# Performance work log

Measured on AMD Instinct MI355X. Metric: run time of the kernel, lower is better.

## Reference

```python
import jax, jax.numpy as jnp
import numpy as np

B, C, H = 256, 5, 13
N_AGENTS = 8192
N_EDGES = 262144
ACT = 21


def setup_inputs() -> dict:
    key = jax.random.key(0)
    ks = jax.random.split(key, 20)
    inp = {
        "x": jax.random.normal(ks[0], (B, C, H, H), jnp.float32),
        "x_msg": jax.random.normal(ks[1], (N_AGENTS,), jnp.float32),
        "edge_index": jax.random.randint(ks[2], (N_EDGES, 2), 0, N_AGENTS, jnp.int64 if jax.config.jax_enable_x64 else jnp.int32),
        "action": jax.random.randint(ks[3], (B,), 0, ACT, jnp.int32),
        # params (orthogonal init approximated by scaled normal; math identical)
        "conv1_w": jax.random.normal(ks[4], (32, 5, 3, 3), jnp.float32) * 0.1,
        "conv1_b": jnp.zeros((32,), jnp.float32),
        "conv2_w": jax.random.normal(ks[5], (64, 32, 3, 3), jnp.float32) * 0.05,
        "conv2_b": jnp.zeros((64,), jnp.float32),
        "fc_w": jax.random.normal(ks[6], (512, 1024), jnp.float32) * 0.03,
        "fc_b": jnp.zeros((512,), jnp.float32),
        "fc_mu_w": jax.random.normal(ks[7], (ACT, 512), jnp.float32) * 0.01,
        "fc_mu_b": jnp.zeros((ACT,), jnp.float32),
        "msg_w": jax.random.normal(ks[8], (N_AGENTS, 512), jnp.float32) * 0.01,
        "msg_b": jnp.zeros((N_AGENTS,), jnp.float32),
        "gcn1_w": jax.random.normal(ks[9], (2, 16), jnp.float32) * 0.5,
        "gcn1_b": jnp.zeros((16,), jnp.float32),
        "gcn2_w": jax.random.normal(ks[10], (16, N_AGENTS), jnp.float32) * 0.1,
        "gcn2_b": jnp.zeros((N_AGENTS,), jnp.float32),
    }
    return inp


def _gcn_norm(edge_index, n):
    # add self-loops; edge_index is (E,2) [src, dst]
    loops = jnp.arange(n, dtype=edge_index.dtype)
    src = jnp.concatenate([edge_index[:, 0], loops])
    dst = jnp.concatenate([edge_index[:, 1], loops])
    deg = jax.ops.segment_sum(jnp.ones_like(src, jnp.float32), dst, num_segments=n)
    dinv = jnp.where(deg > 0, jax.lax.rsqrt(deg), 0.0)
    norm = dinv[src] * dinv[dst]  # [E+n]
    return src, dst, norm


def _gcn_conv(h, src, dst, norm, W, b, n):
    hw = h @ W  # [n, out]
    out = jax.ops.segment_sum(norm[:, None] * hw[src], dst, num_segments=n)
    return out + b


def reference(x, x_msg, edge_index, action, conv1_w, conv1_b, conv2_w, conv2_b,
              fc_w, fc_b, fc_mu_w, fc_mu_b, msg_w, msg_b,
              gcn1_w, gcn1_b, gcn2_w, gcn2_b):
    dn = ("NCHW", "OIHW", "NCHW")
    h = jax.lax.conv_general_dilated(x, conv1_w, (2, 2), "VALID", dimension_numbers=dn)
    h = jax.nn.relu(h + conv1_b[None, :, None, None])  # [B,32,6,6]
    h = jax.lax.conv_general_dilated(h, conv2_w, (1, 1), "VALID", dimension_numbers=dn)
    h = jax.nn.relu(h + conv2_b[None, :, None, None])  # [B,64,4,4]
    h = h.reshape(h.shape[0], -1)  # [B,1024], torch NCHW flatten order
    hidden = jax.nn.relu(h @ fc_w.T + fc_b)  # [B,512]

    logits = hidden @ fc_mu_w.T + fc_mu_b            # [B,21]
    actor_encoding = hidden @ msg_w.T + msg_b        # [B,N]

    # Categorical log_prob / entropy for the given action
    logp = jax.nn.log_softmax(logits, axis=-1)
    log_prob = jnp.take_along_axis(logp, action[:, None], axis=1)[:, 0]
    entropy = -jnp.sum(jnp.exp(logp) * logp, axis=-1)

    # GNN message branch (eval mode: dropout is identity)
    feats = jnp.stack([x_msg, actor_encoding[0]], axis=0).T  # [N,2]
    n = feats.shape[0]
    src, dst, norm = _gcn_norm(edge_index, n)
    g = jax.nn.relu(_gcn_conv(feats, src, dst, norm, gcn1_w, gcn1_b, n))  # [N,16]
    g = _gcn_conv(g, src, dst, norm, gcn2_w, gcn2_b, n)                    # [N,N]
    msg_out = jax.nn.log_softmax(g, axis=1).mean(axis=1)                   # [N]

    return (action, msg_out, log_prob, entropy)
```

## Files before the change

kernel.cpp:

```cpp
#include <hip/hip_runtime.h>
#include <hip/hip_bf16.h>

#define NB 256
#define NACT 21
#define NA 8192
#define NE 262144
#define CSR_CAP 128
#define LOG2E 1.44269504f

#if __has_builtin(__builtin_amdgcn_exp2f)
#define EXP2F(x) __builtin_amdgcn_exp2f(x)
#else
#define EXP2F(x) exp2f(x)
#endif

typedef __attribute__((ext_vector_type(8))) short short8;
typedef __attribute__((ext_vector_type(4))) float float4v;

__device__ inline float wsum64(float v) {
#pragma unroll
  for (int m = 32; m > 0; m >>= 1) v += __shfl_xor(v, m, 64);
  return v;
}

__device__ inline unsigned short f2bf(float f) {
  union { __hip_bfloat16 h; unsigned short u; } cv;
  cv.h = __float2bfloat16(f);
  return cv.u;
}

__global__ __launch_bounds__(512) void k_init(int* cnt) {
  int i = blockIdx.x * 512 + threadIdx.x;
  cnt[i] = 0;
}

__global__ __launch_bounds__(512, 2) void k_pc(
    const int* __restrict__ edges, const float* __restrict__ fcw,
    const float* __restrict__ g2w, const float* __restrict__ g2b,
    unsigned short* fcwbf, unsigned short* w2t, float* wpart, int* cnt, int* csr,
    const float* __restrict__ x, const float* __restrict__ c1w, const float* __restrict__ c1b,
    const float* __restrict__ c2w, const float* __restrict__ c2b, unsigned short* h1024bf) {
  __shared__ float sm[8109];
  int t = threadIdx.x;
  if (blockIdx.x < 512) {
    float (*red)[17] = (float(*)[17])sm;
    float* b2s = sm + 272;
    int blk = blockIdx.x;
    {
      int e = blk * 512 + t;
      int s = edges[2 * e], d = edges[2 * e + 1];
      int slot = atomicAdd(&cnt[d], 1);
      if (slot < CSR_CAP) csr[d * CSR_CAP + slot] = s;
    }
    {
      int base = (blk * 512 + t) * 2;
      float2 v = *(const float2*)&fcw[base];
      fcwbf[base + 0] = f2bf(v.x);
      fcwbf[base + 1] = f2bf(v.y);
    }
    {
      if (t < 256) {
        int jj = t >> 4, k = t & 15;
        int j = blk * 16 + jj;
        float w = g2w[k * 8192 + j];
        w2t[j * 16 + k] = f2bf(w);
        red[jj][k] = w;
      }
      if (t < 16) b2s[t] = g2b[blk * 16 + t];
      __syncthreads();
      if (t < 16) {
        float s = 0.0f;
#pragma unroll
        for (int q = 0; q < 16; q++) s += red[q][t];
        wpart[blk * 17 + t] = s;
      } else if (t == 16) {
        float s = 0.0f;
#pragma unroll
        for (int q = 0; q < 16; q++) s += b2s[q];
        wpart[blk * 17 + 16] = s;
      }
    }
  } else {
    float* xs = sm;
    float* w1s = sm + 845;
    float* c1s = sm + 2285;
    float* w2s = sm + 3437;
    int blk = blockIdx.x - 512;
    for (int i = t; i < 845; i += 512) xs[i] = x[blk * 845 + i];
    for (int i = t; i < 1440; i += 512) w1s[i] = c1w[i];
    __syncthreads();
    for (int idx = t; idx < 1152; idx += 512) {
      int oc = idx / 36, p = idx - oc * 36;
      int oy = p / 6, ox = p - oy * 6;
      float acc = c1b[oc];
      const float* wp = &w1s[oc * 45];
#pragma unroll
      for (int ic = 0; ic < 5; ic++)
#pragma unroll
        for (int ky = 0; ky < 3; ky++)
#pragma unroll
          for (int kx = 0; kx < 3; kx++)
            acc += xs[ic * 169 + (oy * 2 + ky) * 13 + ox * 2 + kx] * wp[ic * 9 + ky * 3 + kx];
      c1s[idx] = fmaxf(acc, 0.0f);
    }
    int p = t & 15, oc2 = t >> 4;
    int oy = p >> 2, ox = p & 3;
    float a0 = c2b[oc2 * 2 + 0], a1 = c2b[oc2 * 2 + 1];
    for (int icb = 0; icb < 32; icb += 8) {
      __syncthreads();
      for (int i = t; i < 4608; i += 512) {
        int oc = i / 72, r = i - oc * 72;
        w2s[oc * 73 + r] = c2w[oc * 288 + icb * 9 + r];
      }
      __syncthreads();
#pragma unroll
      for (int ic = 0; ic < 8; ic++) {
#pragma unroll
        for (int ky = 0; ky < 3; ky++) {
#pragma unroll
          for (int kx = 0; kx < 3; kx++) {
            float cvv = c1s[(icb + ic) * 36 + (oy + ky) * 6 + ox + kx];
            int wi = ic * 9 + ky * 3 + kx;
            a0 += cvv * w2s[(oc2 * 2 + 0) * 73 + wi];
            a1 += cvv * w2s[(oc2 * 2 + 1) * 73 + wi];
          }
        }
      }
    }
    unsigned short* hp = &h1024bf[blk * 1024];
    hp[(oc2 * 2 + 0) * 16 + p] = f2bf(fmaxf(a0, 0.0f));
    hp[(oc2 * 2 + 1) * 16 + p] = f2bf(fmaxf(a1, 0.0f));
  }
}

__global__ __launch_bounds__(256, 4) void k_fc(
    const int* __restrict__ cnt, const float* __restrict__ x_msg,
    const unsigned short* __restrict__ h1024bf, const unsigned short* __restrict__ fcwbf,
    const float* __restrict__ fcb, const float* __restrict__ wpart,
    float* hidden, float* dinv, float* xs2, float* wsf) {
  __shared__ float red[4][256];
  int t = threadIdx.x, blk = blockIdx.x;
  if (blk == 512) {
    if (t < 17) {
      float s = 0.0f;
      for (int b = 0; b < 512; b++) s += wpart[b * 17 + t];
      wsf[t] = s;
    }
    return;
  }
  int wave = t >> 6, lane = t & 63;
  if (blk < 32) {
    int i = blk * 256 + t;
    float d = rsqrtf((float)cnt[i] + 1.0f);
    dinv[i] = d;
    xs2[i] = d * x_msg[i];
  }
  int tr = blk >> 5, tc = blk & 31;
  int m = lane & 15, quad = lane >> 4;
  const unsigned short* ap = &h1024bf[(tr * 16 + m) * 1024 + wave * 256 + quad * 8];
  const unsigned short* bp = &fcwbf[(tc * 16 + m) * 1024 + wave * 256 + quad * 8];
  float4v acc = {0.0f, 0.0f, 0.0f, 0.0f};
#pragma unroll
  for (int i = 0; i < 8; i++) {
    short8 a = *(const short8*)(ap + i * 32);
    short8 b = *(const short8*)(bp + i * 32);
    acc = __builtin_amdgcn_mfma_f32_16x16x32_bf16(a, b, acc, 0, 0, 0);
  }
#pragma unroll
  for (int r = 0; r < 4; r++) red[wave][(quad * 4 + r) * 16 + m] = acc[r];
  __syncthreads();
  {
    float s = red[0][t] + red[1][t] + red[2][t] + red[3][t];
    int gr = tr * 16 + (t >> 4);
    int gc = tc * 16 + (t & 15);
    hidden[gr * 512 + gc] = fmaxf(s + fcb[gc], 0.0f);
  }
}

__global__ __launch_bounds__(512, 2) void k_he(
    const float* __restrict__ hidden, const float* __restrict__ muw,
    const float* __restrict__ mub, const float* __restrict__ msgw,
    const float* __restrict__ msgb, const float* __restrict__ dinv,
    const int* __restrict__ action, float* es2, float* out) {
  __shared__ float muT[10752];
  __shared__ float hrows[2048];
  int t = threadIdx.x, blk = blockIdx.x;
  int wave = t >> 6, lane = t & 63;
  if (blk < 64) {
    int b0 = blk * 4;
    for (int i = t; i < 10752; i += 512) {
      int a = i >> 9, k = i & 511;
      muT[k * 21 + a] = muw[i];
    }
    for (int i = t; i < 2048; i += 512) hrows[i] = hidden[b0 * 512 + i];
    __syncthreads();
    if (wave < 4) {
      int b = b0 + wave;
      float logit = -1e30f;
      if (lane < NACT) {
        float acc = mub[lane];
        const float* hr = &hrows[wave * 512];
        for (int k = 0; k < 512; k++) acc += hr[k] * muT[k * 21 + lane];
        logit = acc;
      }
      float m = logit;
#pragma unroll
      for (int s = 32; s > 0; s >>= 1) m = fmaxf(m, __shfl_xor(m, s, 64));
      float e = (lane < NACT) ? __expf(logit - m) : 0.0f;
      float se = wsum64(e);
      float swl = wsum64(e * logit);
      float lse = m + __logf(se);
      int act = action[b];
      if (lane == 0) {
        out[b] = (float)act;
        out[8704 + b] = lse - swl / se;
      }
      if (lane == act) out[8448 + b] = logit - lse;
    }
  } else {
    int wg = (blk - 64) * 8 + wave;
    for (int j = wg; j < NA; j += 3584) {
      const float* wp = &msgw[j * 512 + lane * 8];
      float4 w0 = *(const float4*)(wp);
      float4 w1 = *(const float4*)(wp + 4);
      float4 h0 = *(const float4*)&hidden[lane * 8];
      float4 h1 = *(const float4*)&hidden[lane * 8 + 4];
      float s = w0.x * h0.x + w0.y * h0.y + w0.z * h0.z + w0.w * h0.w +
                w1.x * h1.x + w1.y * h1.y + w1.z * h1.z + w1.w * h1.w;
      s = wsum64(s);
      if (lane == 0) es2[j] = dinv[j] * (s + msgb[j]);
    }
  }
}

__global__ __launch_bounds__(512, 4) void k_g1(
    const int* __restrict__ cnt, const int* __restrict__ csr,
    const float* __restrict__ dinv, const float* __restrict__ xs2,
    const float* __restrict__ es2, const float* __restrict__ g1w,
    const float* __restrict__ g1b, float* gbuf2) {
  int t = threadIdx.x, blk = blockIdx.x;
  int wave = t >> 6, lane = t & 63;
  int wg = blk * 8 + wave;
#pragma unroll
  for (int rr = 0; rr < 2; rr++) {
    int i = wg * 2 + rr;
    int ci = min(cnt[i], CSR_CAP);
    float di = dinv[i];
    float a0 = 0.0f, a1 = 0.0f;
    for (int e = lane; e < ci; e += 64) {
      int s = csr[i * CSR_CAP + e];
      a0 += xs2[s];
      a1 += es2[s];
    }
    float f0 = (wsum64(a0) + xs2[i]) * di;
    float f1 = (wsum64(a1) + es2[i]) * di;
    if (lane < 16) {
      float gv = fmaxf(f0 * g1w[lane] + f1 * g1w[16 + lane] + g1b[lane], 0.0f);
      gbuf2[i * 16 + lane] = di * gv;
    }
  }
}

__global__ __launch_bounds__(512, 2) void k_msg(
    const int* __restrict__ cnt, const int* __restrict__ csr,
    const float* __restrict__ dinv, const float* __restrict__ gbuf2,
    const float* __restrict__ wsf, const unsigned short* __restrict__ w2t,
    const float* __restrict__ g2b, float* out) {
  __shared__ __align__(16) unsigned short vbf[256];
  __shared__ float vf[256];
  __shared__ float pl[2048];
  __shared__ float sl[128];
  __shared__ float wsfs[17];
  int t = threadIdx.x, blk = blockIdx.x;
  int wave = t >> 6, lane = t & 63;
  int rowbase = blk * 16;
  if (t < 17) wsfs[t] = wsf[t];
  {
    int eq = lane >> 4, c = lane & 15;
#pragma unroll
    for (int rr = 0; rr < 2; rr++) {
      int il = wave * 2 + rr;
      int i = rowbase + il;
      int ci = min(cnt[i], CSR_CAP);
      float di = dinv[i];
      float acc = (eq == 0) ? gbuf2[i * 16 + c] : 0.0f;
      for (int e = eq; e < ci; e += 4) {
        int s = csr[i * CSR_CAP + e];
        acc += gbuf2[s * 16 + c];
      }
      acc *= di;
      acc += __shfl_xor(acc, 16, 64);
      acc += __shfl_xor(acc, 32, 64);
      if (eq == 0) {
        vf[il * 16 + c] = acc;
        vbf[il * 16 + c] = f2bf(acc * LOG2E);
      }
    }
  }
  __syncthreads();
  float myMean = 0.0f;
  if (t < 16) {
    float dot = 0.0f;
#pragma unroll
    for (int c = 0; c < 16; c++) dot += vf[t * 16 + c] * wsfs[c];
    myMean = (dot + wsfs[16]) * (1.0f / 8192.0f);
  }
  {
    int quad = lane >> 4, n = lane & 15;
    int k8 = quad * 8;
    short8 za = {0, 0, 0, 0, 0, 0, 0, 0};
    short8 a1 = za;
    if (quad < 2) a1 = *(const short8*)&vbf[n * 16 + k8];
    float sacc[4];
#pragma unroll
    for (int q = 0; q < 4; q++) sacc[q] = 0.0f;
    int colb = wave * 1024 + n;
    for (int tp = 0; tp < 64; tp += 2) {
      int col1 = colb + tp * 16;
      int col2 = col1 + 16;
      short8 b1 = za, b2 = za;
      if (quad < 2) {
        b1 = *(const short8*)&w2t[col1 * 16 + k8];
        b2 = *(const short8*)&w2t[col2 * 16 + k8];
      }
      float bb1 = g2b[col1] * LOG2E, bb2 = g2b[col2] * LOG2E;
      float4v c1 = {bb1, bb1, bb1, bb1};
      float4v c2 = {bb2, bb2, bb2, bb2};
      float4v s11 = __builtin_amdgcn_mfma_f32_16x16x32_bf16(a1, b1, c1, 0, 0, 0);
      float4v s12 = __builtin_amdgcn_mfma_f32_16x16x32_bf16(a1, b2, c2, 0, 0, 0);
#pragma unroll
      for (int r = 0; r < 4; r++) sacc[r] += EXP2F(s11[r]) + EXP2F(s12[r]);
    }
#pragma unroll
    for (int q = 0; q < 4; q++) {
      int rl = quad * 4 + q;
      pl[rl * 128 + wave * 16 + n] = sacc[q];
    }
  }
  __syncthreads();
  if (t < 128) {
    int r = t >> 3, seg = t & 7;
    int base = r * 128 + seg * 16;
    float ll = 0.0f;
#pragma unroll
    for (int i = 0; i < 16; i++) ll += pl[base + i];
    sl[r * 8 + seg] = ll;
  }
  __syncthreads();
  if (t < 16) {
    float ll = 0.0f;
#pragma unroll
    for (int i = 0; i < 8; i++) ll += sl[t * 8 + i];
    out[256 + rowbase + t] = myMean - __logf(ll);
  }
}

extern "C" void kernel_launch(void* const* d_in, const int* in_sizes, int n_in,
                              void* d_out, int out_size, void* d_ws, size_t ws_size,
                              hipStream_t stream) {
  const float* x     = (const float*)d_in[0];
  const float* x_msg = (const float*)d_in[1];
  const int*   edges = (const int*)d_in[2];
  const int*   action= (const int*)d_in[3];
  const float* c1w   = (const float*)d_in[4];
  const float* c1b   = (const float*)d_in[5];
  const float* c2w   = (const float*)d_in[6];
  const float* c2b   = (const float*)d_in[7];
  const float* fcw   = (const float*)d_in[8];
  const float* fcb   = (const float*)d_in[9];
  const float* muw   = (const float*)d_in[10];
  const float* mub   = (const float*)d_in[11];
  const float* msgw  = (const float*)d_in[12];
  const float* msgb  = (const float*)d_in[13];
  const float* g1w   = (const float*)d_in[14];
  const float* g1b   = (const float*)d_in[15];
  const float* g2w   = (const float*)d_in[16];
  const float* g2b   = (const float*)d_in[17];
  float* out = (float*)d_out;

  float* ws     = (float*)d_ws;
  unsigned short* h1024bf = (unsigned short*)ws;
  unsigned short* fcwbf   = (unsigned short*)(ws + 131072);
  float* hidden = ws + 393216;
  float* es2    = ws + 524288;
  float* dinv   = ws + 532480;
  float* xs2    = ws + 540672;
  float* gbuf2  = ws + 548864;
  float* wpart  = ws + 679936;
  unsigned short* w2t = (unsigned short*)(ws + 688640);
  int*   cnt    = (int*)(ws + 754176);
  int*   csr    = (int*)(ws + 762368);
  float* wsf    = ws + 1810944;

  k_init<<<16, 512, 0, stream>>>(cnt);
  k_pc <<<768, 512, 0, stream>>>(edges, fcw, g2w, g2b, fcwbf, w2t, wpart, cnt, csr,
                                 x, c1w, c1b, c2w, c2b, h1024bf);
  k_fc <<<513, 256, 0, stream>>>(cnt, x_msg, h1024bf, fcwbf, fcb, wpart, hidden, dinv, xs2, wsf);
  k_he <<<512, 512, 0, stream>>>(hidden, muw, mub, msgw, msgb, dinv, action, es2, out);
  k_g1 <<<512, 512, 0, stream>>>(cnt, csr, dinv, xs2, es2, g1w, g1b, gbuf2);
  k_msg<<<512, 512, 0, stream>>>(cnt, csr, dinv, gbuf2, wsf, w2t, g2b, out);
}
```

Before: 183.7 us.

## Split conv blocks per image into two halves, reorder blocks, parallelize wpart reduction

The conv2 stage now uses two blocks per image, each computing 32 output channels with one accumulator per thread, and these conv blocks are scheduled before the edge/CSR blocks. Shared memory per block shrinks, which may allow more resident blocks. Conv1 is recomputed redundantly in both halves. The final 512-row wpart reduction in k_fc is split across 272 threads with a shared-memory second stage instead of 17 serial threads.

```diff
diff --git a/kernel.cpp b/kernel.cpp
--- a/kernel.cpp
+++ b/kernel.cpp
@@ -40,12 +40,12 @@
     unsigned short* fcwbf, unsigned short* w2t, float* wpart, int* cnt, int* csr,
     const float* __restrict__ x, const float* __restrict__ c1w, const float* __restrict__ c1b,
     const float* __restrict__ c2w, const float* __restrict__ c2b, unsigned short* h1024bf) {
-  __shared__ float sm[8109];
+  __shared__ float sm[5773];
   int t = threadIdx.x;
-  if (blockIdx.x < 512) {
+  if (blockIdx.x >= 512) {
     float (*red)[17] = (float(*)[17])sm;
     float* b2s = sm + 272;
-    int blk = blockIdx.x;
+    int blk = blockIdx.x - 512;
     {
       int e = blk * 512 + t;
       int s = edges[2 * e], d = edges[2 * e + 1];
@@ -85,8 +85,8 @@
     float* w1s = sm + 845;
     float* c1s = sm + 2285;
     float* w2s = sm + 3437;
-    int blk = blockIdx.x - 512;
-    for (int i = t; i < 845; i += 512) xs[i] = x[blk * 845 + i];
+    int img = blockIdx.x >> 1, half = blockIdx.x & 1;
+    for (int i = t; i < 845; i += 512) xs[i] = x[img * 845 + i];
     for (int i = t; i < 1440; i += 512) w1s[i] = c1w[i];
     __syncthreads();
     for (int idx = t; idx < 1152; idx += 512) {
@@ -103,14 +103,15 @@
             acc += xs[ic * 169 + (oy * 2 + ky) * 13 + ox * 2 + kx] * wp[ic * 9 + ky * 3 + kx];
       c1s[idx] = fmaxf(acc, 0.0f);
     }
-    int p = t & 15, oc2 = t >> 4;
+    int p = t & 15, ocl = t >> 4;
     int oy = p >> 2, ox = p & 3;
-    float a0 = c2b[oc2 * 2 + 0], a1 = c2b[oc2 * 2 + 1];
+    int oc = half * 32 + ocl;
+    float a0 = c2b[oc];
     for (int icb = 0; icb < 32; icb += 8) {
       __syncthreads();
-      for (int i = t; i < 4608; i += 512) {
-        int oc = i / 72, r = i - oc * 72;
-        w2s[oc * 73 + r] = c2w[oc * 288 + icb * 9 + r];
+      for (int i = t; i < 2304; i += 512) {
+        int o = i / 72, r = i - o * 72;
+        w2s[o * 73 + r] = c2w[(half * 32 + o) * 288 + icb * 9 + r];
       }
       __syncthreads();
 #pragma unroll
@@ -120,16 +121,12 @@
 #pragma unroll
           for (int kx = 0; kx < 3; kx++) {
             float cvv = c1s[(icb + ic) * 36 + (oy + ky) * 6 + ox + kx];
-            int wi = ic * 9 + ky * 3 + kx;
-            a0 += cvv * w2s[(oc2 * 2 + 0) * 73 + wi];
-            a1 += cvv * w2s[(oc2 * 2 + 1) * 73 + wi];
+            a0 += cvv * w2s[ocl * 73 + ic * 9 + ky * 3 + kx];
           }
         }
       }
     }
-    unsigned short* hp = &h1024bf[blk * 1024];
-    hp[(oc2 * 2 + 0) * 16 + p] = f2bf(fmaxf(a0, 0.0f));
-    hp[(oc2 * 2 + 1) * 16 + p] = f2bf(fmaxf(a1, 0.0f));
+    h1024bf[img * 1024 + oc * 16 + p] = f2bf(fmaxf(a0, 0.0f));
   }
 }
 
@@ -141,9 +138,18 @@
   __shared__ float red[4][256];
   int t = threadIdx.x, blk = blockIdx.x;
   if (blk == 512) {
+    float* part = &red[0][0];
+    if (t < 272) {
+      int q = t / 17, c = t - q * 17;
+      float s = 0.0f;
+      for (int r = q; r < 512; r += 16) s += wpart[r * 17 + c];
+      part[t] = s;
+    }
+    __syncthreads();
     if (t < 17) {
       float s = 0.0f;
-      for (int b = 0; b < 512; b++) s += wpart[b * 17 + t];
+#pragma unroll
+      for (int q = 0; q < 16; q++) s += part[q * 17 + t];
       wsf[t] = s;
     }
     return;
@@ -393,8 +399,8 @@
   float* wsf    = ws + 1810944;
 
   k_init<<<16, 512, 0, stream>>>(cnt);
-  k_pc <<<768, 512, 0, stream>>>(edges, fcw, g2w, g2b, fcwbf, w2t, wpart, cnt, csr,
-                                 x, c1w, c1b, c2w, c2b, h1024bf);
+  k_pc <<<1024, 512, 0, stream>>>(edges, fcw, g2w, g2b, fcwbf, w2t, wpart, cnt, csr,
+                                  x, c1w, c1b, c2w, c2b, h1024bf);
   k_fc <<<513, 256, 0, stream>>>(cnt, x_msg, h1024bf, fcwbf, fcb, wpart, hidden, dinv, xs2, wsf);
   k_he <<<512, 512, 0, stream>>>(hidden, muw, mub, msgw, msgb, dinv, action, es2, out);
   k_g1 <<<512, 512, 0, stream>>>(cnt, csr, dinv, xs2, es2, g1w, g1b, gbuf2);
```

Measured after the change: 242.7 us. 1.32x slower.
